# Performance work log

Hardware: AMD Instinct MI355X
Metric: run time of the kernel (lower is better)

## Reference

```python
import jax, jax.numpy as jnp
import numpy as np

B, T, H, DK, DV, HID = 2, 2048, 6, 256, 256, 2048
EPS = 1e-5


def setup_inputs() -> dict:
    key = jax.random.key(0)
    ks = jax.random.split(key, 12)
    sd = 0.02
    hidden_ab = jax.random.normal(ks[0], (B, T, HID), jnp.float32)
    hidden_g = jax.random.normal(ks[1], (B, T, HID), jnp.float32)
    q = jax.random.normal(ks[2], (B, T, H, DK), jnp.float32)
    k = jax.random.normal(ks[3], (B, T, H, DK), jnp.float32)
    v = jax.random.normal(ks[4], (B, T, H, DV), jnp.float32)
    b_w = jax.random.normal(ks[5], (H, HID), jnp.float32) * sd
    a_w = jax.random.normal(ks[6], (H, HID), jnp.float32) * sd
    g_w = jax.random.normal(ks[7], (H, HID), jnp.float32) * sd
    A_log = jnp.log(jax.random.uniform(ks[8], (H,), jnp.float32, 1.0, 16.0))
    dt = jnp.exp(jax.random.uniform(ks[9], (H,), jnp.float32)
                 * (np.log(0.1) - np.log(0.001)) + np.log(0.001))
    dt = jnp.clip(dt, 1e-4)
    dt_bias = dt + jnp.log(-jnp.expm1(-dt))
    norm_w = jnp.ones((DV,), jnp.float32)
    o_w = jax.random.normal(ks[10], (H, DV, DK), jnp.float32) * sd
    return dict(hidden_ab=hidden_ab, hidden_g=hidden_g, q=q, k=k, v=v,
                b_w=b_w, a_w=a_w, A_log=A_log, dt_bias=dt_bias,
                g_w=g_w, norm_w=norm_w, o_w=o_w)


def _l2norm(x):
    return x * jax.lax.rsqrt(jnp.sum(x * x, axis=-1, keepdims=True) + 1e-6)


def _gated_delta_rule(q, k, v, g, beta):
    # q,k: [B,T,H,DK]; v: [B,T,H,DV]; g,beta: [B,T,H]
    q = _l2norm(q) * (DK ** -0.5)
    k = _l2norm(k)
    # time-major for scan
    qT = jnp.swapaxes(q, 0, 1)
    kT = jnp.swapaxes(k, 0, 1)
    vT = jnp.swapaxes(v, 0, 1)
    gT = jnp.swapaxes(g, 0, 1)
    bT = jnp.swapaxes(beta, 0, 1)

    def step(S, xs):
        qt, kt, vt, gt, bt = xs  # [B,H,*]
        S = S * jnp.exp(gt)[..., None, None]            # gated decay
        pred = jnp.einsum('bhk,bhkv->bhv', kt, S)        # current prediction
        delta = (vt - pred) * bt[..., None]              # beta-scaled error
        S = S + jnp.einsum('bhk,bhv->bhkv', kt, delta)   # delta-rule update
        ot = jnp.einsum('bhk,bhkv->bhv', qt, S)
        return S, ot

    S0 = jnp.zeros((B, H, DK, DV), q.dtype)
    _, oT = jax.lax.scan(step, S0, (qT, kT, vT, gT, bT))
    return jnp.swapaxes(oT, 0, 1)  # [B,T,H,DV]


def reference(hidden_ab, hidden_g, q, k, v, b_w, a_w, A_log, dt_bias, g_w, norm_w, o_w):
    beta = jax.nn.sigmoid(jnp.einsum('bth,nh->btn', hidden_ab, b_w))        # [B,T,H]
    g = -jnp.exp(A_log) * jax.nn.softplus(
        jnp.einsum('bth,nh->btn', hidden_ab, a_w) + dt_bias)                 # [B,T,H]
    o = _gated_delta_rule(q, k, v, g, beta)                                  # [B,T,H,DV]
    # FusedRMSNormSwishGate with per-head scalar gate
    gate = jnp.einsum('bth,nh->btn', hidden_g, g_w)                          # [B,T,H]
    o_n = o * jax.lax.rsqrt(jnp.mean(o * o, axis=-1, keepdims=True) + EPS) * norm_w
    o_n = o_n * (gate * jax.nn.sigmoid(gate))[..., None]
    # GroupLinear per head: head_v_dim -> head_dim
    out = jnp.einsum('bthv,hvd->bthd', o_n, o_w).reshape(B, T, H * DK)
    return out
```

## Files before the change

kernel.cpp:

```cpp
#include <hip/hip_runtime.h>
#include <hip/hip_bf16.h>
#include <math.h>

#define B_ 2
#define T_ 2048
#define H_ 6
#define DK_ 256
#define DV_ 256
#define HID_ 2048
#define C_ 64
#define NC_ 32

typedef __attribute__((ext_vector_type(8))) short short8;
typedef __attribute__((ext_vector_type(4))) float f32x4;

__device__ __forceinline__ unsigned rnebf(float f) {
  unsigned u = __float_as_uint(f);
  return (u + 0x7fffu + ((u >> 16) & 1u)) >> 16;
}
__device__ __forceinline__ unsigned pkbf(float lo, float hi) {
  return rnebf(lo) | (rnebf(hi) << 16);
}
__device__ __forceinline__ float bf2f(unsigned u16v) {
  return __uint_as_float((u16v & 0xffffu) << 16);
}
__device__ __forceinline__ short8 u4_to_s8(uint4 u) {
  union { uint4 u; short8 s; } c; c.u = u; return c.s;
}

__device__ __forceinline__ void gload_lds16(const void* g, void* l) {
  __builtin_amdgcn_global_load_lds(
      (const __attribute__((address_space(1))) unsigned int*)g,
      (__attribute__((address_space(3))) unsigned int*)l, 16, 0, 0);
}

__device__ __forceinline__ short8 buildB(uint2 Pe, uint2 Po, int lg, int c16) {
  const int src0 = ((2 * (lg & 1)) << 4) | c16;
  const int src1 = src0 + 16;
  int e0 = __shfl((int)Pe.x, src0), o0 = __shfl((int)Po.x, src0);
  int e1 = __shfl((int)Pe.y, src0), o1 = __shfl((int)Po.y, src0);
  int e2 = __shfl((int)Pe.x, src1), o2 = __shfl((int)Po.x, src1);
  int e3 = __shfl((int)Pe.y, src1), o3 = __shfl((int)Po.y, src1);
  const bool lo2 = (lg < 2);
  union { int i[4]; short8 s; } u;
  u.i[0] = lo2 ? e0 : o0;
  u.i[1] = lo2 ? e1 : o1;
  u.i[2] = lo2 ? e2 : o2;
  u.i[3] = lo2 ? e3 : o3;
  return u.s;
}

__global__ __launch_bounds__(256) void gdn_proj_kernel(
    const float* __restrict__ hab, const float* __restrict__ hg,
    const float* __restrict__ b_w, const float* __restrict__ a_w,
    const float* __restrict__ g_w, const float* __restrict__ A_log,
    const float* __restrict__ dt_bias,
    float* __restrict__ beta_o, float* __restrict__ g_o,
    float* __restrict__ sgate_o) {
  const int bt = blockIdx.x;
  const int tid = threadIdx.x;
  const int lane = tid & 63;
  const int wid = tid >> 6;

  const float* h1 = hab + (size_t)bt * HID_ + tid * 8;
  const float* h2 = hg + (size_t)bt * HID_ + tid * 8;
  const float4 xa = *(const float4*)(h1);
  const float4 xb = *(const float4*)(h1 + 4);
  const float4 ya = *(const float4*)(h2);
  const float4 yb = *(const float4*)(h2 + 4);

  float part[18];
#pragma unroll
  for (int n = 0; n < 6; ++n) {
    const float* wp = b_w + n * HID_ + tid * 8;
    const float4 w0 = *(const float4*)(wp);
    const float4 w1 = *(const float4*)(wp + 4);
    part[n] = xa.x * w0.x + xa.y * w0.y + xa.z * w0.z + xa.w * w0.w +
              xb.x * w1.x + xb.y * w1.y + xb.z * w1.z + xb.w * w1.w;
  }
#pragma unroll
  for (int n = 0; n < 6; ++n) {
    const float* wp = a_w + n * HID_ + tid * 8;
    const float4 w0 = *(const float4*)(wp);
    const float4 w1 = *(const float4*)(wp + 4);
    part[6 + n] = xa.x * w0.x + xa.y * w0.y + xa.z * w0.z + xa.w * w0.w +
                  xb.x * w1.x + xb.y * w1.y + xb.z * w1.z + xb.w * w1.w;
  }
#pragma unroll
  for (int n = 0; n < 6; ++n) {
    const float* wp = g_w + n * HID_ + tid * 8;
    const float4 w0 = *(const float4*)(wp);
    const float4 w1 = *(const float4*)(wp + 4);
    part[12 + n] = ya.x * w0.x + ya.y * w0.y + ya.z * w0.z + ya.w * w0.w +
                   yb.x * w1.x + yb.y * w1.y + yb.z * w1.z + yb.w * w1.w;
  }

  __shared__ float red[18][4];
#pragma unroll
  for (int i = 0; i < 18; ++i) {
    float x = part[i];
    x += __shfl_xor(x, 1);
    x += __shfl_xor(x, 2);
    x += __shfl_xor(x, 4);
    x += __shfl_xor(x, 8);
    x += __shfl_xor(x, 16);
    x += __shfl_xor(x, 32);
    if (lane == 0) red[i][wid] = x;
  }
  __syncthreads();

  if (tid < 18) {
    const float s = red[tid][0] + red[tid][1] + red[tid][2] + red[tid][3];
    if (tid < 6) {
      beta_o[(size_t)bt * H_ + tid] = 1.f / (1.f + __expf(-s));
    } else if (tid < 12) {
      const int n = tid - 6;
      const float x = s + dt_bias[n];
      const float sp = (x > 20.f) ? x : log1pf(__expf(x));
      g_o[(size_t)bt * H_ + n] = -__expf(A_log[n]) * sp;
    } else {
      const int n = tid - 12;
      sgate_o[(size_t)bt * H_ + n] = s / (1.f + __expf(-s));
    }
  }
}

__global__ __launch_bounds__(256) void gdn_cum_kernel(
    const float* __restrict__ g, float* __restrict__ Gc,
    float* __restrict__ lam) {
  const int bh = blockIdx.x;
  const int b = bh / H_, h = bh - b * H_;
  const int w = threadIdx.x >> 6, l = threadIdx.x & 63;
  for (int it = 0; it < 8; ++it) {
    const int nc = it * 4 + w;
    const int tg = nc * C_ + l;
    const size_t srow = ((size_t)b * T_ + tg) * H_ + h;
    float val = g[srow];
#pragma unroll
    for (int ofs = 1; ofs < 64; ofs <<= 1) {
      const float o = __shfl_up(val, ofs);
      if (l >= ofs) val += o;
    }
    Gc[(bh * NC_ + nc) * C_ + l] = val;
    if (l == 63) lam[bh * NC_ + nc] = __expf(val);
  }
}

__global__ __launch_bounds__(256, 1) void gdn_prep_kernel(
    const float* __restrict__ q, const float* __restrict__ k,
    const float* __restrict__ v, const float* __restrict__ beta,
    const float* __restrict__ Gc, uint2* __restrict__ wUp,
    ushort* __restrict__ wWp, ushort* __restrict__ wMp,
    ushort* __restrict__ wQd, ushort* __restrict__ wkT,
    const float* __restrict__ o_w, ushort* __restrict__ owT) {
  __shared__ __attribute__((aligned(16))) char smem[94464];

  const int bid = blockIdx.x;
  const int tid = threadIdx.x;

  if (bid >= 512) {
    const int b2 = bid - 512;
    const int h2 = b2 >> 2;
    const int db = (b2 & 3) * 64;
    ushort* t = (ushort*)smem;
#pragma unroll
    for (int it = 0; it < 16; ++it) {
      const int v2 = it * 16 + (tid >> 4);
      const int dl = 4 * (tid & 15);
      const float4 x =
          *(const float4*)&o_w[((size_t)h2 * 256 + v2) * 256 + db + dl];
      t[(dl + 0) * 264 + v2] = (ushort)rnebf(x.x);
      t[(dl + 1) * 264 + v2] = (ushort)rnebf(x.y);
      t[(dl + 2) * 264 + v2] = (ushort)rnebf(x.z);
      t[(dl + 3) * 264 + v2] = (ushort)rnebf(x.w);
    }
    __syncthreads();
#pragma unroll
    for (int it = 0; it < 8; ++it) {
      const int idx = it * 256 + tid;
      const int d = idx >> 5;
      const int vv = (idx & 31) * 8;
      uint4 o;
      o.x = *(uint*)&t[d * 264 + vv + 0]; o.y = *(uint*)&t[d * 264 + vv + 2];
      o.z = *(uint*)&t[d * 264 + vv + 4]; o.w = *(uint*)&t[d * 264 + vv + 6];
      *(uint4*)&owT[((size_t)h2 * 256 + db + d) * 256 + vv] = o;
    }
    return;
  }

  const int bhx = bid & 15;
  if (bhx >= B_ * H_) return;
  const int nc = bid >> 4;
  const int bh = bhx;
  const int b = bh / H_, h = bh - b * H_;
  const int w = tid >> 6, l = tid & 63;
  const int lg = l >> 4, c16 = l & 15;
  const int cidx = bh * NC_ + nc;

  ushort* knB = (ushort*)smem;
  ushort* qnB = (ushort*)(smem + 32768);
  float* AlT = (float*)(smem + 65536);
  ushort* Msc = (ushort*)(smem + 82944);
  float* bG = (float*)(smem + 92160);
  float* bB = bG + 64;
  float* bSc = bG + 128;
  float* bWl = bG + 192;
  float* bKg = bG + 256;
  float* bQg = bG + 320;
  float* bSk = bG + 384;
  float* bSq = bG + 448;
  float* bQe = bG + 512;

  const size_t srow0 = ((size_t)b * T_ + nc * C_) * H_ + h;
  if (tid < C_) {
    bG[tid] = Gc[cidx * C_ + tid];
    bB[tid] = beta[srow0 + (size_t)tid * H_];
  }
  __syncthreads();

#pragma unroll
  for (int rr = 0; rr < 16; ++rr) {
    const int row = rr * 4 + w;
    const size_t g0 = (srow0 + (size_t)row * H_) * DK_;
    const float4 kv = *(const float4*)(k + g0 + 4 * l);
    const float4 qv = *(const float4*)(q + g0 + 4 * l);
    const int boff = row * 512 + ((8 * l) ^ ((row & 7) << 4));
    uint2 pk_, pq_;
    pk_.x = pkbf(kv.x, kv.y); pk_.y = pkbf(kv.z, kv.w);
    pq_.x = pkbf(qv.x, qv.y); pq_.y = pkbf(qv.z, qv.w);
    *(uint2*)((char*)knB + boff) = pk_;
    *(uint2*)((char*)qnB + boff) = pq_;
  }
  __syncthreads();

  f32x4 accm[4], acca[4];
  {
    const int xorv = (c16 & 7) << 4;
    const int rowA = 16 * w + c16;
    uint4 aq[8], ak[8];
#pragma unroll
    for (int kt = 0; kt < 8; ++kt) {
      const int coff = (64 * kt + 16 * lg) ^ xorv;
      aq[kt] = *(const uint4*)((char*)qnB + rowA * 512 + coff);
      ak[kt] = *(const uint4*)((char*)knB + rowA * 512 + coff);
    }
#pragma unroll
    for (int nt = 0; nt < 4; ++nt) {
      accm[nt] = (f32x4){0.f, 0.f, 0.f, 0.f};
      acca[nt] = (f32x4){0.f, 0.f, 0.f, 0.f};
    }
    f32x4 accq = (f32x4){0.f, 0.f, 0.f, 0.f};
#pragma unroll
    for (int nt = 0; nt < 4; ++nt) {
      const int rowB = 16 * nt + c16;
#pragma unroll
      for (int kt = 0; kt < 8; ++kt) {
        const uint4 bk =
            *(const uint4*)((char*)knB + rowB * 512 + ((64 * kt + 16 * lg) ^ xorv));
        const short8 bkf = u4_to_s8(bk);
        accm[nt] = __builtin_amdgcn_mfma_f32_16x16x32_bf16(u4_to_s8(aq[kt]),
                                                           bkf, accm[nt], 0, 0, 0);
        acca[nt] = __builtin_amdgcn_mfma_f32_16x16x32_bf16(u4_to_s8(ak[kt]),
                                                           bkf, acca[nt], 0, 0, 0);
      }
    }
#pragma unroll
    for (int kt = 0; kt < 8; ++kt) {
      const short8 bq = u4_to_s8(aq[kt]);
      accq = __builtin_amdgcn_mfma_f32_16x16x32_bf16(bq, bq, accq, 0, 0, 0);
    }
#pragma unroll
    for (int r = 0; r < 4; ++r) {
      if ((c16 >> 2) == lg && (c16 & 3) == r) {
        bKg[16 * w + c16] = acca[w][r];
        bQg[16 * w + c16] = accq[r];
      }
    }
  }
  __syncthreads();

  if (tid < C_) {
    const float gv = bG[tid];
    const float gend = bG[C_ - 1];
    const float skv = rsqrtf(bKg[tid] + 1e-6f);
    const float sqv = rsqrtf(bQg[tid] + 1e-6f) * 0.0625f;
    bSk[tid] = skv;
    bSq[tid] = sqv;
    bSc[tid] = __expf(gend - gv) * skv;
    bWl[tid] = bB[tid] * __expf(gv) * skv;
    bQe[tid] = sqv * __expf(gv);
  }
  __syncthreads();

  {
#pragma unroll
    for (int nt = 0; nt < 4; ++nt) {
#pragma unroll
      for (int r = 0; r < 4; ++r) {
        const int t = 16 * w + 4 * lg + r;
        const int i = 16 * nt + c16;
        const float eg = __expf(bG[t] - bG[i]);
        const float ski = bSk[i];
        Msc[t * 72 + i] =
            (ushort)((i <= t) ? rnebf(accm[nt][r] * bSq[t] * ski * eg) : 0u);
        AlT[i * 68 + t] =
            (i < t) ? bB[t] * bSk[t] * ski * eg * acca[nt][r] : 0.f;
      }
    }
  }
  float xw[64];
  {
    const int d = tid;
#pragma unroll
    for (int e = 0; e < 8; ++e) {
      float vj[8];
#pragma unroll
      for (int j = 0; j < 8; ++j) {
        const int t = 8 * e + j;
        const float kv = bf2f(*(const ushort*)((char*)knB + t * 512 +
                                               ((2 * d) ^ ((t & 7) << 4))));
        vj[j] = kv;
        xw[t] = kv * bWl[t];
      }
      uint4 o;
      o.x = pkbf(vj[0] * bSc[8 * e + 0], vj[1] * bSc[8 * e + 1]);
      o.y = pkbf(vj[2] * bSc[8 * e + 2], vj[3] * bSc[8 * e + 3]);
      o.z = pkbf(vj[4] * bSc[8 * e + 4], vj[5] * bSc[8 * e + 5]);
      o.w = pkbf(vj[6] * bSc[8 * e + 6], vj[7] * bSc[8 * e + 7]);
      *(uint4*)&wkT[((size_t)cidx * 256 + d) * C_ + 8 * e] = o;
    }
  }
#pragma unroll
  for (int rr = 0; rr < 16; ++rr) {
    const int row = rr * 4 + w;
    const float qe = bQe[row];
    const uint2 pq =
        *(const uint2*)((char*)qnB + row * 512 + ((8 * l) ^ ((row & 7) << 4)));
    const float q0 = bf2f(pq.x), q1 = bf2f(pq.x >> 16);
    const float q2 = bf2f(pq.y), q3 = bf2f(pq.y >> 16);
    uint2 oq;
    oq.x = pkbf(q0 * qe, q1 * qe);
    oq.y = pkbf(q2 * qe, q3 * qe);
    *(uint2*)&wQd[(srow0 + (size_t)row * H_) * DK_ + 4 * l] = oq;
  }
  __syncthreads();

  {
    const int row = tid >> 2;
#pragma unroll
    for (int e = 0; e < 2; ++e) {
      const int col = ((tid & 3) * 2 + e) * 8;
      *(uint4*)&wMp[(size_t)cidx * C_ * C_ + row * C_ + col] =
          *(const uint4*)&Msc[row * 72 + col];
    }
  }
  float xu[64];
#pragma unroll
  for (int t = 0; t < C_; ++t)
    xu[t] = v[(srow0 + (size_t)t * H_) * DV_ + tid] * bB[t];

#pragma unroll
  for (int tb = 0; tb < 8; ++tb) {
#pragma unroll
    for (int i = 0; i < 8 * tb; ++i) {
      const float xui = xu[i];
      const float xwi = xw[i];
      float av[8];
      *(float4*)&av[0] = *(float4*)&AlT[i * 68 + 8 * tb];
      *(float4*)&av[4] = *(float4*)&AlT[i * 68 + 8 * tb + 4];
#pragma unroll
      for (int e = 0; e < 8; ++e) {
        xu[8 * tb + e] = fmaf(-av[e], xui, xu[8 * tb + e]);
        xw[8 * tb + e] = fmaf(-av[e], xwi, xw[8 * tb + e]);
      }
    }
#pragma unroll
    for (int e = 1; e < 8; ++e)
#pragma unroll
      for (int m = 0; m < 7; ++m)
        if (m < e) {
          const float am = AlT[(8 * tb + m) * 68 + 8 * tb + e];
          xu[8 * tb + e] = fmaf(-am, xu[8 * tb + m], xu[8 * tb + e]);
          xw[8 * tb + e] = fmaf(-am, xw[8 * tb + m], xw[8 * tb + e]);
        }
  }
  {
    ushort* wb = wWp + (size_t)cidx * C_ * 256;
#pragma unroll
    for (int row = 0; row < C_; ++row)
      wb[row * 256 + tid] = (ushort)rnebf(xw[row]);
    const int cbw = tid >> 4, c16s = tid & 15;
#pragma unroll
    for (int mt = 0; mt < 4; ++mt) {
#pragma unroll
      for (int lgi = 0; lgi < 4; ++lgi) {
        const int r0 = 16 * mt + 4 * lgi;
        uint2 val;
        val.x = pkbf(xu[r0 + 0], xu[r0 + 1]);
        val.y = pkbf(xu[r0 + 2], xu[r0 + 3]);
        wUp[(((size_t)cidx * 16 + cbw) * 4 + mt) * 64 + (lgi << 4) + c16s] = val;
      }
    }
  }
}

__global__ __launch_bounds__(128, 1) void gdn_seq_kernel(
    const ushort* __restrict__ wkT, const ushort* __restrict__ wWp,
    const uint2* __restrict__ wUp, const float* __restrict__ lam,
    uint2* __restrict__ wDP, uint2* __restrict__ wSP) {
  const int bid = blockIdx.x;
  const int cb = bid >> 4, bhx = bid & 15;
  if (bhx >= B_ * H_) return;
  const int bh = bhx;
  const int tid = threadIdx.x;
  const int kh = tid >> 6, l = tid & 63;
  const int lg = l >> 4, c16 = l & 15;
  const int xorv = (c16 & 7) << 4;

  __shared__ ushort sW[2][16384];
  __shared__ ushort sK[2][16384];
  __shared__ uint2 sU[2][256];
  __shared__ f32x4 sX[2][4][64];
  __shared__ float sLam[NC_];

  auto stage = [&](int pp, int cidx2) {
    const char* gw_ = (const char*)(wWp + (size_t)cidx2 * 16384);
#pragma unroll
    for (int j = 0; j < 16; ++j) {
      const int i = kh * 16 + j;
      const int row = 2 * i + (l >> 5);
      const int colb = ((l & 31) * 16) ^ ((row & 7) << 4);
      gload_lds16(gw_ + row * 512 + colb, (char*)&sW[pp][0] + i * 1024);
    }
    const char* gk_ = (const char*)(wkT + (size_t)cidx2 * 16384);
#pragma unroll
    for (int j = 0; j < 16; ++j) {
      const int i = kh * 16 + j;
      const int row = 8 * i + (l >> 3);
      const int colb = ((l & 7) * 16) ^ ((row & 7) << 4);
      gload_lds16(gk_ + row * 128 + colb, (char*)&sK[pp][0] + i * 1024);
    }
    const char* gu_ = (const char*)wUp + ((size_t)cidx2 * 16 + cb) * 2048;
    gload_lds16(gu_ + kh * 1024 + l * 16, (char*)&sU[pp][0] + kh * 1024);
  };

  f32x4 S[8];
#pragma unroll
  for (int m2 = 0; m2 < 8; ++m2) S[m2] = (f32x4){0.f, 0.f, 0.f, 0.f};

  stage(0, bh * NC_ + 0);
  stage(1, bh * NC_ + 1);
  if (tid < NC_) sLam[tid] = lam[bh * NC_ + tid];
  asm volatile("s_waitcnt lgkmcnt(0)" ::: "memory");
  __builtin_amdgcn_sched_barrier(0);
  __builtin_amdgcn_s_barrier();
  __builtin_amdgcn_sched_barrier(0);

  for (int nc = 0; nc < NC_; ++nc) {
    const int pp = nc & 1;
    const int cidx = bh * NC_ + nc;
    if (nc == 0)
      asm volatile("s_waitcnt vmcnt(33)" ::: "memory");
    else if (nc == NC_ - 1)
      asm volatile("s_waitcnt vmcnt(5)" ::: "memory");
    else
      asm volatile("s_waitcnt vmcnt(38)" ::: "memory");
    __builtin_amdgcn_sched_barrier(0);
    __builtin_amdgcn_s_barrier();
    __builtin_amdgcn_sched_barrier(0);

    uint2 P[8];
#pragma unroll
    for (int m2 = 0; m2 < 8; ++m2) {
      P[m2].x = pkbf(S[m2][0], S[m2][1]);
      P[m2].y = pkbf(S[m2][2], S[m2][3]);
    }
    {
      uint4* sp4 = (uint4*)(wSP + (((size_t)cidx * 16 + cb) * 64 + l) * 16 +
                            kh * 8);
#pragma unroll
      for (int i = 0; i < 4; ++i) {
        uint4 o; o.x = P[2 * i].x; o.y = P[2 * i].y;
        o.z = P[2 * i + 1].x; o.w = P[2 * i + 1].y;
        sp4[i] = o;
      }
    }

    f32x4 pe[4], po[4];
#pragma unroll
    for (int mt = 0; mt < 4; ++mt) {
      pe[mt] = (f32x4){0.f, 0.f, 0.f, 0.f};
      po[mt] = (f32x4){0.f, 0.f, 0.f, 0.f};
    }
    const char* sWb = (const char*)&sW[pp][0];
#pragma unroll
    for (int ktl = 0; ktl < 4; ++ktl) {
      const int kt = kh * 4 + ktl;
      const short8 Bf = buildB(P[2 * ktl], P[2 * ktl + 1], lg, c16);
      const int colb = (64 * kt + 16 * lg) ^ xorv;
#pragma unroll
      for (int mt = 0; mt < 4; ++mt) {
        const uint4 aw = *(const uint4*)(sWb + (16 * mt + c16) * 512 + colb);
        if (ktl & 1)
          po[mt] = __builtin_amdgcn_mfma_f32_16x16x32_bf16(u4_to_s8(aw), Bf,
                                                           po[mt], 0, 0, 0);
        else
          pe[mt] = __builtin_amdgcn_mfma_f32_16x16x32_bf16(u4_to_s8(aw), Bf,
                                                           pe[mt], 0, 0, 0);
      }
    }
    f32x4 pl[4];
#pragma unroll
    for (int mt = 0; mt < 4; ++mt) {
      pl[mt] = pe[mt] + po[mt];
      sX[kh][mt][l] = pl[mt];
    }
    asm volatile("s_waitcnt lgkmcnt(0)" ::: "memory");
    __builtin_amdgcn_sched_barrier(0);
    __builtin_amdgcn_s_barrier();
    __builtin_amdgcn_sched_barrier(0);

    uint2 DP[4];
#pragma unroll
    for (int mt = 0; mt < 4; ++mt) {
      const f32x4 pr = sX[kh ^ 1][mt][l];
      const uint2 uu = sU[pp][mt * 64 + l];
      const float d0 = bf2f(uu.x) - (pl[mt][0] + pr[0]);
      const float d1 = bf2f(uu.x >> 16) - (pl[mt][1] + pr[1]);
      const float d2 = bf2f(uu.y) - (pl[mt][2] + pr[2]);
      const float d3 = bf2f(uu.y >> 16) - (pl[mt][3] + pr[3]);
      DP[mt].x = pkbf(d0, d1);
      DP[mt].y = pkbf(d2, d3);
    }
    {
      uint4* dp4 = (uint4*)(wDP + (((size_t)cidx * 16 + cb) * 64 + l) * 4);
      uint4 od;
      if (kh == 0) { od.x = DP[0].x; od.y = DP[0].y; od.z = DP[1].x; od.w = DP[1].y; }
      else         { od.x = DP[2].x; od.y = DP[2].y; od.z = DP[3].x; od.w = DP[3].y; }
      dp4[kh] = od;
    }
    const float lamC = sLam[nc];
#pragma unroll
    for (int m2 = 0; m2 < 8; ++m2) {
      S[m2][0] *= lamC; S[m2][1] *= lamC; S[m2][2] *= lamC; S[m2][3] *= lamC;
    }
    const char* sKb = (const char*)&sK[pp][0];
#pragma unroll
    for (int kt2 = 0; kt2 < 2; ++kt2) {
      const short8 Bd = buildB(DP[2 * kt2], DP[2 * kt2 + 1], lg, c16);
      const int colb = (64 * kt2 + 16 * lg) ^ xorv;
#pragma unroll
      for (int m2 = 0; m2 < 8; ++m2) {
        const int m2g = kh * 8 + m2;
        const uint4 ak = *(const uint4*)(sKb + (16 * m2g + c16) * 128 + colb);
        S[m2] = __builtin_amdgcn_mfma_f32_16x16x32_bf16(u4_to_s8(ak), Bd,
                                                        S[m2], 0, 0, 0);
      }
    }
    __builtin_amdgcn_sched_barrier(0);
    __builtin_amdgcn_s_barrier();
    __builtin_amdgcn_sched_barrier(0);
    if (nc + 2 < NC_) stage(pp, cidx + 2);
    __builtin_amdgcn_sched_barrier(0);
  }
}

__global__ __launch_bounds__(256) void gdn_ofin_kernel(
    const ushort* __restrict__ wQd, const ushort* __restrict__ wMp,
    const uint2* __restrict__ wDP, const uint2* __restrict__ wSP,
    const float* __restrict__ sgate, const float* __restrict__ norm_w,
    const ushort* __restrict__ owT, float* __restrict__ out) {
  const int slot = blockIdx.x;
  const int bhx = slot & 15;
  if (bhx >= B_ * H_) return;
  const int nc = slot >> 4;
  const int bh = bhx;
  const int cidx = bh * NC_ + nc;
  const int b = bh / H_, h = bh - b * H_;
  const int tid = threadIdx.x;
  const int w = tid >> 6, l = tid & 63;
  const int lg = l >> 4, c16 = l & 15;
  const size_t t0 = (size_t)b * T_ + nc * C_;

  __shared__ ushort onl[64 * 256];
  __shared__ float red[64][4];
  __shared__ float rowf[64];

  f32x4 acc[4][4];
#pragma unroll
  for (int mt = 0; mt < 4; ++mt)
#pragma unroll
    for (int nt = 0; nt < 4; ++nt) acc[mt][nt] = (f32x4){0.f, 0.f, 0.f, 0.f};

#pragma unroll
  for (int nt = 0; nt < 4; ++nt) {
    const int cbwq = 4 * w + nt;
    uint2 SPl[16];
    const uint4* sp4 =
        (const uint4*)(wSP + (((size_t)cidx * 16 + cbwq) * 64 + l) * 16);
#pragma unroll
    for (int i = 0; i < 8; ++i) {
      const uint4 t4 = sp4[i];
      SPl[2 * i].x = t4.x; SPl[2 * i].y = t4.y;
      SPl[2 * i + 1].x = t4.z; SPl[2 * i + 1].y = t4.w;
    }
#pragma unroll
    for (int kt = 0; kt < 8; ++kt) {
      const short8 Bf = buildB(SPl[2 * kt], SPl[2 * kt + 1], lg, c16);
#pragma unroll
      for (int mt = 0; mt < 4; ++mt) {
        const uint4 aq = *(const uint4*)&wQd[((t0 + 16 * mt + c16) * H_ + h) *
                                                 (size_t)DK_ +
                                             32 * kt + 8 * lg];
        acc[mt][nt] = __builtin_amdgcn_mfma_f32_16x16x32_bf16(
            u4_to_s8(aq), Bf, acc[mt][nt], 0, 0, 0);
      }
    }
  }
  const ushort* Mb = wMp + (size_t)cidx * C_ * C_;
#pragma unroll
  for (int nt = 0; nt < 4; ++nt) {
    const int cbwq = 4 * w + nt;
    uint2 DPl[4];
    {
      const uint4* dp4 =
          (const uint4*)(wDP + (((size_t)cidx * 16 + cbwq) * 64 + l) * 4);
      const uint4 a0 = dp4[0], a1 = dp4[1];
      DPl[0].x = a0.x; DPl[0].y = a0.y; DPl[1].x = a0.z; DPl[1].y = a0.w;
      DPl[2].x = a1.x; DPl[2].y = a1.y; DPl[3].x = a1.z; DPl[3].y = a1.w;
    }
#pragma unroll
    for (int kt2 = 0; kt2 < 2; ++kt2) {
      const short8 Bf = buildB(DPl[2 * kt2], DPl[2 * kt2 + 1], lg, c16);
#pragma unroll
      for (int mt = 0; mt < 4; ++mt) {
        const uint4 am =
            *(const uint4*)&Mb[(16 * mt + c16) * C_ + 32 * kt2 + 8 * lg];
        acc[mt][nt] = __builtin_amdgcn_mfma_f32_16x16x32_bf16(
            u4_to_s8(am), Bf, acc[mt][nt], 0, 0, 0);
      }
    }
  }

  float ss[4][4];
#pragma unroll
  for (int mt = 0; mt < 4; ++mt)
#pragma unroll
    for (int r = 0; r < 4; ++r) {
      float s = acc[mt][0][r] * acc[mt][0][r];
      s = fmaf(acc[mt][1][r], acc[mt][1][r], s);
      s = fmaf(acc[mt][2][r], acc[mt][2][r], s);
      s = fmaf(acc[mt][3][r], acc[mt][3][r], s);
      s += __shfl_xor(s, 1);
      s += __shfl_xor(s, 2);
      s += __shfl_xor(s, 4);
      s += __shfl_xor(s, 8);
      ss[mt][r] = s;
    }
  if (c16 == 0) {
#pragma unroll
    for (int mt = 0; mt < 4; ++mt)
#pragma unroll
      for (int r = 0; r < 4; ++r) red[16 * mt + 4 * lg + r][w] = ss[mt][r];
  }
  __syncthreads();
  if (tid < 64) {
    const float ms =
        (red[tid][0] + red[tid][1] + red[tid][2] + red[tid][3]) * (1.f / DV_);
    const float sg = sgate[(t0 + tid) * H_ + h];
    rowf[tid] = rsqrtf(ms + 1e-5f) * sg;
  }
  __syncthreads();

  {
    char* onb = (char*)onl;
#pragma unroll
    for (int mt = 0; mt < 4; ++mt) {
      float rf[4];
#pragma unroll
      for (int r = 0; r < 4; ++r) rf[r] = rowf[16 * mt + 4 * lg + r];
#pragma unroll
      for (int nt = 0; nt < 4; ++nt) {
        const int c = (4 * w + nt) * 16 + c16;
        const float nwv = norm_w[c];
#pragma unroll
        for (int r = 0; r < 4; ++r) {
          const int row = 16 * mt + 4 * lg + r;
          const float v = acc[mt][nt][r] * rf[r] * nwv;
          *(ushort*)(onb + row * 512 + ((2 * c) ^ ((row & 7) << 4))) =
              (ushort)rnebf(v);
        }
      }
    }
  }
  __syncthreads();

  f32x4 acc2[4][4];
#pragma unroll
  for (int mt = 0; mt < 4; ++mt)
#pragma unroll
    for (int nt2 = 0; nt2 < 4; ++nt2)
      acc2[mt][nt2] = (f32x4){0.f, 0.f, 0.f, 0.f};
  {
    const char* onb = (const char*)onl;
#pragma unroll
    for (int kt = 0; kt < 8; ++kt) {
      uint4 af[4];
#pragma unroll
      for (int mt = 0; mt < 4; ++mt)
        af[mt] = *(const uint4*)(onb + (16 * mt + c16) * 512 +
                                 ((64 * kt + 16 * lg) ^ ((c16 & 7) << 4)));
#pragma unroll
      for (int nt2 = 0; nt2 < 4; ++nt2) {
        const uint4 bf = *(const uint4*)&owT[((size_t)h * 256 +
                                              (4 * w + nt2) * 16 + c16) *
                                                 256 +
                                             32 * kt + 8 * lg];
#pragma unroll
        for (int mt = 0; mt < 4; ++mt)
          acc2[mt][nt2] = __builtin_amdgcn_mfma_f32_16x16x32_bf16(
              u4_to_s8(af[mt]), u4_to_s8(bf), acc2[mt][nt2], 0, 0, 0);
      }
    }
  }
#pragma unroll
  for (int mt = 0; mt < 4; ++mt)
#pragma unroll
    for (int nt2 = 0; nt2 < 4; ++nt2)
#pragma unroll
      for (int r = 0; r < 4; ++r)
        out[((t0 + 16 * mt + 4 * lg + r) * H_ + h) * (size_t)DK_ +
            (4 * w + nt2) * 16 + c16] = acc2[mt][nt2][r];
}

extern "C" void kernel_launch(void* const* d_in, const int* in_sizes, int n_in,
                              void* d_out, int out_size, void* d_ws,
                              size_t ws_size, hipStream_t stream) {
  const float* hab = (const float*)d_in[0];
  const float* hg = (const float*)d_in[1];
  const float* q = (const float*)d_in[2];
  const float* k = (const float*)d_in[3];
  const float* v = (const float*)d_in[4];
  const float* b_w = (const float*)d_in[5];
  const float* a_w = (const float*)d_in[6];
  const float* A_log = (const float*)d_in[7];
  const float* dt_bias = (const float*)d_in[8];
  const float* g_w = (const float*)d_in[9];
  const float* norm_w = (const float*)d_in[10];
  const float* o_w = (const float*)d_in[11];
  float* out = (float*)d_out;

  float* ws = (float*)d_ws;
  const size_t NBT = (size_t)B_ * T_ * H_;
  float* w_beta = ws;
  float* w_g = ws + NBT;
  float* w_sg = ws + 2 * NBT;
  float* w_G = ws + 5 * NBT;
  float* w_lam = ws + 7 * NBT;
  ushort* w_Qd = (ushort*)(ws + 7 * NBT + 1024);
  ushort* w_kT = w_Qd + (size_t)12582912;
  ushort* w_W = w_kT + (size_t)6291456;
  ushort* w_M = w_W + (size_t)6291456;
  uint2* w_U = (uint2*)(w_M + (size_t)1572864);
  uint2* w_DP = w_U + (size_t)1572864;
  uint2* w_SP = w_DP + (size_t)1572864;
  ushort* w_owT = (ushort*)(w_SP + (size_t)6291456);

  hipLaunchKernelGGL(gdn_proj_kernel, dim3(B_ * T_), dim3(256), 0, stream,
                     hab, hg, b_w, a_w, g_w, A_log, dt_bias, w_beta, w_g,
                     w_sg);
  hipLaunchKernelGGL(gdn_cum_kernel, dim3(B_ * H_), dim3(256), 0, stream,
                     w_g, w_G, w_lam);
  hipLaunchKernelGGL(gdn_prep_kernel, dim3(512 + 24), dim3(256), 0, stream,
                     q, k, v, w_beta, w_G, w_U, w_W, w_M, w_Qd, w_kT, o_w,
                     w_owT);
  hipLaunchKernelGGL(gdn_seq_kernel, dim3(256), dim3(128), 0, stream,
                     w_kT, w_W, w_U, w_lam, w_DP, w_SP);
  hipLaunchKernelGGL(gdn_ofin_kernel, dim3(512), dim3(256), 0, stream,
                     w_Qd, w_M, w_DP, w_SP, w_sg, norm_w, w_owT, out);
}
```

Measured before the change: 256.2 us.

## Split prep kernel into MFMA stage and forward-substitution stage via global workspace

Splits the chunk prep kernel into two launches. The first computes the attention-like matrices with MFMA and writes the A-lower matrix and pre-scaled k (W) to global memory. The second reloads them and runs the triangular forward substitution to produce U and W. This lowers register and LDS pressure per kernel and drops the one-block-per-CU launch bound. In exchange it adds an extra launch, a global round trip for AlT and W, and an extra bf16 rounding of W before the substitution.

```diff
diff --git a/kernel.cpp b/kernel.cpp
--- a/kernel.cpp
+++ b/kernel.cpp
@@ -146,14 +146,14 @@
   }
 }
 
-__global__ __launch_bounds__(256, 1) void gdn_prep_kernel(
+__global__ __launch_bounds__(256) void gdn_prep_mfma_kernel(
     const float* __restrict__ q, const float* __restrict__ k,
-    const float* __restrict__ v, const float* __restrict__ beta,
-    const float* __restrict__ Gc, uint2* __restrict__ wUp,
+    const float* __restrict__ beta, const float* __restrict__ Gc,
     ushort* __restrict__ wWp, ushort* __restrict__ wMp,
     ushort* __restrict__ wQd, ushort* __restrict__ wkT,
+    float* __restrict__ wAlT, float* __restrict__ wScl,
     const float* __restrict__ o_w, ushort* __restrict__ owT) {
-  __shared__ __attribute__((aligned(16))) char smem[94464];
+  __shared__ __attribute__((aligned(16))) char smem[77312];
 
   const int bid = blockIdx.x;
   const int tid = threadIdx.x;
@@ -199,9 +199,8 @@
 
   ushort* knB = (ushort*)smem;
   ushort* qnB = (ushort*)(smem + 32768);
-  float* AlT = (float*)(smem + 65536);
-  ushort* Msc = (ushort*)(smem + 82944);
-  float* bG = (float*)(smem + 92160);
+  ushort* Msc = (ushort*)(smem + 65536);
+  float* bG = (float*)(smem + 74752);
   float* bB = bG + 64;
   float* bSc = bG + 128;
   float* bWl = bG + 192;
@@ -293,6 +292,7 @@
   __syncthreads();
 
   {
+    float* gA = wAlT + (size_t)cidx * 4096;
 #pragma unroll
     for (int nt = 0; nt < 4; ++nt) {
 #pragma unroll
@@ -303,14 +303,14 @@
         const float ski = bSk[i];
         Msc[t * 72 + i] =
             (ushort)((i <= t) ? rnebf(accm[nt][r] * bSq[t] * ski * eg) : 0u);
-        AlT[i * 68 + t] =
+        gA[i * 64 + t] =
             (i < t) ? bB[t] * bSk[t] * ski * eg * acca[nt][r] : 0.f;
       }
     }
   }
-  float xw[64];
   {
     const int d = tid;
+    ushort* wb = wWp + (size_t)cidx * C_ * 256;
 #pragma unroll
     for (int e = 0; e < 8; ++e) {
       float vj[8];
@@ -320,7 +320,7 @@
         const float kv = bf2f(*(const ushort*)((char*)knB + t * 512 +
                                                ((2 * d) ^ ((t & 7) << 4))));
         vj[j] = kv;
-        xw[t] = kv * bWl[t];
+        wb[t * 256 + d] = (ushort)rnebf(kv * bWl[t]);
       }
       uint4 o;
       o.x = pkbf(vj[0] * bSc[8 * e + 0], vj[1] * bSc[8 * e + 1]);
@@ -354,6 +354,42 @@
           *(const uint4*)&Msc[row * 72 + col];
     }
   }
+  (void)wScl;
+}
+
+__global__ __launch_bounds__(256) void gdn_prep_fs_kernel(
+    const float* __restrict__ v, const float* __restrict__ beta,
+    const float* __restrict__ wAlT, ushort* __restrict__ wWp,
+    uint2* __restrict__ wUp) {
+  __shared__ __attribute__((aligned(16))) float AlT[64 * 68];
+  __shared__ float bB[64];
+
+  const int slot = blockIdx.x;
+  const int bhx = slot & 15;
+  if (bhx >= B_ * H_) return;
+  const int nc = slot >> 4;
+  const int bh = bhx;
+  const int b = bh / H_, h = bh - b * H_;
+  const int tid = threadIdx.x;
+  const int cidx = bh * NC_ + nc;
+  const size_t srow0 = ((size_t)b * T_ + nc * C_) * H_ + h;
+
+  {
+    const float* gA = wAlT + (size_t)cidx * 4096;
+#pragma unroll
+    for (int it = 0; it < 16; ++it) {
+      const int idx = it * 256 + tid;
+      AlT[(idx >> 6) * 68 + (idx & 63)] = gA[idx];
+    }
+  }
+  if (tid < C_) bB[tid] = beta[srow0 + (size_t)tid * H_];
+  __syncthreads();
+
+  float xw[64];
+  ushort* wb = wWp + (size_t)cidx * C_ * 256;
+#pragma unroll
+  for (int t = 0; t < C_; ++t) xw[t] = bf2f(wb[t * 256 + tid]);
+
   float xu[64];
 #pragma unroll
   for (int t = 0; t < C_; ++t)
@@ -385,7 +421,6 @@
         }
   }
   {
-    ushort* wb = wWp + (size_t)cidx * C_ * 256;
 #pragma unroll
     for (int row = 0; row < C_; ++row)
       wb[row * 256 + tid] = (ushort)rnebf(xw[row]);
@@ -765,15 +800,18 @@
   uint2* w_DP = w_U + (size_t)1572864;
   uint2* w_SP = w_DP + (size_t)1572864;
   ushort* w_owT = (ushort*)(w_SP + (size_t)6291456);
+  float* w_AlT = (float*)(w_owT + (size_t)393216);
 
   hipLaunchKernelGGL(gdn_proj_kernel, dim3(B_ * T_), dim3(256), 0, stream,
                      hab, hg, b_w, a_w, g_w, A_log, dt_bias, w_beta, w_g,
                      w_sg);
   hipLaunchKernelGGL(gdn_cum_kernel, dim3(B_ * H_), dim3(256), 0, stream,
                      w_g, w_G, w_lam);
-  hipLaunchKernelGGL(gdn_prep_kernel, dim3(512 + 24), dim3(256), 0, stream,
-                     q, k, v, w_beta, w_G, w_U, w_W, w_M, w_Qd, w_kT, o_w,
-                     w_owT);
+  hipLaunchKernelGGL(gdn_prep_mfma_kernel, dim3(512 + 24), dim3(256), 0,
+                     stream, q, k, w_beta, w_G, w_W, w_M, w_Qd, w_kT, w_AlT,
+                     nullptr, o_w, w_owT);
+  hipLaunchKernelGGL(gdn_prep_fs_kernel, dim3(512), dim3(256), 0, stream,
+                     v, w_beta, w_AlT, w_W, w_U);
   hipLaunchKernelGGL(gdn_seq_kernel, dim3(256), dim3(128), 0, stream,
                      w_kT, w_W, w_U, w_lam, w_DP, w_SP);
   hipLaunchKernelGGL(gdn_ofin_kernel, dim3(512), dim3(256), 0, stream,
```

New measurement: 250.7 us, median of 2. 2.2% less time.
